# Optimization experiments

Measured on AMD Instinct MI355X. Metric: run time of the kernel, lower is better.

## Reference

```python
import jax, jax.numpy as jnp
import numpy as np

N, K, F = 16384, 64, 2048
ALPHA = 1.0
GAMMA = 1.0


def setup_inputs() -> dict:
    key = jax.random.key(0)
    k1, k2, k3, k4 = jax.random.split(key, 4)
    features = jax.random.normal(k1, (N, F), dtype=jnp.float32)
    idx = jax.random.randint(k2, (N,), 0, K)
    labels = jax.nn.one_hot(idx, K, dtype=jnp.float32)  # [N, K] one-hot
    # original initializes clusters to zeros (degenerate); use small random values
    cluster = jax.random.normal(k3, (K, F), dtype=jnp.float32) * 0.02
    class_weight = jax.random.uniform(k4, (K,), dtype=jnp.float32, minval=0.5, maxval=1.5)
    return {"features": features, "labels": labels, "cluster": cluster,
            "class_weight": class_weight}


def reference(features, labels, cluster, class_weight):
    # ci: cluster center of each sample's argmax label  [N, F]
    idx = jnp.argmax(labels, axis=1)
    ci = cluster[idx]
    # numerator: squared distance to own center  [N]
    nume = jnp.sum((features - ci) ** 2, axis=1)
    # denom: sum_j ||c_j - c_i||^2 + alpha  (TF flattens cj to [N, K*F] and
    # tiles ci K times; the squared norm over that axis is exactly this sum)
    d2 = jnp.sum((cluster[:, None, :] - cluster[None, :, :]) ** 2, axis=-1)  # [K, K]
    row_sum = jnp.sum(d2, axis=1)                                            # [K]
    denom = row_sum[idx] + ALPHA                                             # [N]
    loss = (nume / denom)[:, None]                                           # [N, 1]
    # cluster update: weighted_delta[k,f] = sum_n cw[n,k]*labels[n,k]*(x[n,f]-c[k,f])/denom[n]
    # with cw[n,k] = labels[n,k] * class_weight[k]. Expressed without the
    # [N,K,F] intermediates the TF code materializes:
    A = (labels * labels) * class_weight[None, :] / denom[:, None]  # [N, K]
    weighted_delta = jnp.einsum('nk,nf->kf', A, features) - jnp.sum(A, axis=0)[:, None] * cluster
    new_cluster = cluster - GAMMA * weighted_delta  # assign_sub side effect
    return loss, new_cluster
```

## Files before the change

kernel.cpp:

```cpp
#include <hip/hip_runtime.h>

#define NROWS 16384
#define KC 64
#define FDIM 2048
#define F4 (FDIM / 4)
#define ALPHA 1.0f
#define GAMMA 1.0f
#define ROWS_PER_BLK 32
#define HB 256
#define ROWS_PER_HB 64

typedef float f32x4 __attribute__((ext_vector_type(4)));

__global__ __launch_bounds__(256) void k_argmax_hist(
    const float* __restrict__ labels, int* __restrict__ idx,
    int* __restrict__ blockHist) {
    __shared__ int hist[KC];
    int t = threadIdx.x, w = t >> 6, lane = t & 63;
    if (t < KC) hist[t] = 0;
    __syncthreads();
    int rowbase = blockIdx.x * ROWS_PER_HB + w * 16;
    #pragma unroll
    for (int r0 = 0; r0 < 16; r0 += 4) {
        float v0 = labels[(rowbase + r0 + 0) * KC + lane];
        float v1 = labels[(rowbase + r0 + 1) * KC + lane];
        float v2 = labels[(rowbase + r0 + 2) * KC + lane];
        float v3 = labels[(rowbase + r0 + 3) * KC + lane];
        unsigned long long m0 = __ballot(v0 > 0.5f);
        unsigned long long m1 = __ballot(v1 > 0.5f);
        unsigned long long m2 = __ballot(v2 > 0.5f);
        unsigned long long m3 = __ballot(v3 > 0.5f);
        if (lane == 0) {
            int k0 = __ffsll(m0) - 1;
            int k1 = __ffsll(m1) - 1;
            int k2 = __ffsll(m2) - 1;
            int k3 = __ffsll(m3) - 1;
            idx[rowbase + r0 + 0] = k0;
            idx[rowbase + r0 + 1] = k1;
            idx[rowbase + r0 + 2] = k2;
            idx[rowbase + r0 + 3] = k3;
            atomicAdd(&hist[k0], 1);
            atomicAdd(&hist[k1], 1);
            atomicAdd(&hist[k2], 1);
            atomicAdd(&hist[k3], 1);
        }
    }
    __syncthreads();
    if (t < KC) blockHist[blockIdx.x * KC + t] = hist[t];
}

__global__ __launch_bounds__(64) void k_prefix(
    const int* __restrict__ blockHist, int* __restrict__ blockBase,
    int* __restrict__ counts, int* __restrict__ offsets) {
    int k = threadIdx.x;
    int acc = 0;
    for (int b = 0; b < HB; ++b) {
        int c = blockHist[b * KC + k];
        blockBase[b * KC + k] = acc;
        acc += c;
    }
    counts[k] = acc;
    __shared__ int tot[KC];
    tot[k] = acc;
    __syncthreads();
    if (k == 0) {
        int a = 0;
        for (int j = 0; j < KC; ++j) { offsets[j] = a; a += tot[j]; }
    }
}

__global__ __launch_bounds__(64) void k_scatter(
    const int* __restrict__ idx, const int* __restrict__ offsets,
    const int* __restrict__ blockBase, int* __restrict__ order) {
    __shared__ int cur[KC];
    int t = threadIdx.x;
    cur[t] = offsets[t] + blockBase[blockIdx.x * KC + t];
    __syncthreads();
    int n = blockIdx.x * ROWS_PER_HB + t;
    int k = idx[n];
    int p = atomicAdd(&cur[k], 1);
    order[p] = n;
}

__global__ __launch_bounds__(256) void k_rowsum(
    const float* __restrict__ cluster, const float* __restrict__ cw,
    float* __restrict__ inv_denom, float* __restrict__ scale) {
    int k = blockIdx.x, t = threadIdx.x;
    const float4* c4 = (const float4*)cluster;
    float4 a0 = c4[k * F4 + t];
    float4 a1 = c4[k * F4 + 256 + t];
    float acc = 0.f;
    for (int j = 0; j < KC; ++j) {
        float4 b0 = c4[j * F4 + t];
        float4 b1 = c4[j * F4 + 256 + t];
        float d;
        d = a0.x - b0.x; acc += d * d;
        d = a0.y - b0.y; acc += d * d;
        d = a0.z - b0.z; acc += d * d;
        d = a0.w - b0.w; acc += d * d;
        d = a1.x - b1.x; acc += d * d;
        d = a1.y - b1.y; acc += d * d;
        d = a1.z - b1.z; acc += d * d;
        d = a1.w - b1.w; acc += d * d;
    }
    #pragma unroll
    for (int off = 32; off >= 1; off >>= 1) acc += __shfl_down(acc, off);
    __shared__ float red[4];
    if ((t & 63) == 0) red[t >> 6] = acc;
    __syncthreads();
    if (t == 0) {
        float denom = red[0] + red[1] + red[2] + red[3] + ALPHA;
        inv_denom[k] = 1.0f / denom;
        scale[k]     = cw[k] / denom;
    }
}

__global__ __launch_bounds__(256) void k_main(
    const float* __restrict__ features, const float* __restrict__ cluster,
    const int* __restrict__ idx, const int* __restrict__ order,
    const float* __restrict__ inv_denom, float* __restrict__ delta,
    float* __restrict__ loss) {
    int t = threadIdx.x;
    __shared__ float part[ROWS_PER_BLK][256];
    __shared__ int onum[ROWS_PER_BLK];
    __shared__ int okk[ROWS_PER_BLK];
    int base = blockIdx.x * ROWS_PER_BLK;
    if (t < ROWS_PER_BLK) {
        int n = order[base + t];
        onum[t] = n;
        okk[t]  = idx[n];
    }
    __syncthreads();

    const f32x4* f4 = (const f32x4*)features;
    const float4* c4 = (const float4*)cluster;
    int cur_k = -1;
    float4 s0 = {0.f, 0.f, 0.f, 0.f}, s1 = {0.f, 0.f, 0.f, 0.f};
    float4 c0 = s0, c1 = s1;

    for (int r = 0; r < ROWS_PER_BLK; ++r) {
        int n = onum[r];
        int k = okk[r];
        if (k != cur_k) {
            if (cur_k >= 0) {
                float* dk = delta + cur_k * FDIM;
                atomicAdd(&dk[t * 4 + 0], s0.x);
                atomicAdd(&dk[t * 4 + 1], s0.y);
                atomicAdd(&dk[t * 4 + 2], s0.z);
                atomicAdd(&dk[t * 4 + 3], s0.w);
                atomicAdd(&dk[1024 + t * 4 + 0], s1.x);
                atomicAdd(&dk[1024 + t * 4 + 1], s1.y);
                atomicAdd(&dk[1024 + t * 4 + 2], s1.z);
                atomicAdd(&dk[1024 + t * 4 + 3], s1.w);
                s0.x = s0.y = s0.z = s0.w = 0.f;
                s1.x = s1.y = s1.z = s1.w = 0.f;
            }
            c0 = c4[k * F4 + t];
            c1 = c4[k * F4 + 256 + t];
            cur_k = k;
        }
        f32x4 xv0 = __builtin_nontemporal_load(&f4[(size_t)n * F4 + t]);
        f32x4 xv1 = __builtin_nontemporal_load(&f4[(size_t)n * F4 + 256 + t]);
        float4 x0 = {xv0.x, xv0.y, xv0.z, xv0.w};
        float4 x1 = {xv1.x, xv1.y, xv1.z, xv1.w};
        s0.x += x0.x; s0.y += x0.y; s0.z += x0.z; s0.w += x0.w;
        s1.x += x1.x; s1.y += x1.y; s1.z += x1.z; s1.w += x1.w;
        float d, p = 0.f;
        d = x0.x - c0.x; p += d * d;
        d = x0.y - c0.y; p += d * d;
        d = x0.z - c0.z; p += d * d;
        d = x0.w - c0.w; p += d * d;
        d = x1.x - c1.x; p += d * d;
        d = x1.y - c1.y; p += d * d;
        d = x1.z - c1.z; p += d * d;
        d = x1.w - c1.w; p += d * d;
        part[r][t] = p;
    }
    {
        float* dk = delta + cur_k * FDIM;
        atomicAdd(&dk[t * 4 + 0], s0.x);
        atomicAdd(&dk[t * 4 + 1], s0.y);
        atomicAdd(&dk[t * 4 + 2], s0.z);
        atomicAdd(&dk[t * 4 + 3], s0.w);
        atomicAdd(&dk[1024 + t * 4 + 0], s1.x);
        atomicAdd(&dk[1024 + t * 4 + 1], s1.y);
        atomicAdd(&dk[1024 + t * 4 + 2], s1.z);
        atomicAdd(&dk[1024 + t * 4 + 3], s1.w);
    }
    __syncthreads();
    int w = t >> 6, l = t & 63;
    for (int r = w; r < ROWS_PER_BLK; r += 4) {
        float v = part[r][l] + part[r][l + 64] + part[r][l + 128] + part[r][l + 192];
        #pragma unroll
        for (int off = 32; off >= 1; off >>= 1) v += __shfl_down(v, off);
        if (l == 0) {
            loss[onum[r]] = v * inv_denom[okk[r]];
        }
    }
}

__global__ __launch_bounds__(256) void k_finalize(
    const float* __restrict__ cluster, const float* __restrict__ delta,
    const int* __restrict__ counts, const float* __restrict__ scale,
    float* __restrict__ outc) {
    int e = blockIdx.x * 256 + threadIdx.x;
    int k = e >> 9;
    const float4* c4 = (const float4*)cluster;
    const float4* d4 = (const float4*)delta;
    float4 c = c4[e], d = d4[e];
    float s = scale[k], cnt = (float)counts[k];
    float4 o;
    o.x = c.x - GAMMA * s * (d.x - cnt * c.x);
    o.y = c.y - GAMMA * s * (d.y - cnt * c.y);
    o.z = c.z - GAMMA * s * (d.z - cnt * c.z);
    o.w = c.w - GAMMA * s * (d.w - cnt * c.w);
    ((float4*)outc)[e] = o;
}

extern "C" void kernel_launch(void* const* d_in, const int* in_sizes, int n_in,
                              void* d_out, int out_size, void* d_ws, size_t ws_size,
                              hipStream_t stream) {
    const float* features = (const float*)d_in[0];
    const float* labels   = (const float*)d_in[1];
    const float* cluster  = (const float*)d_in[2];
    const float* cw       = (const float*)d_in[3];
    float* loss = (float*)d_out;
    float* outc = (float*)d_out + NROWS;

    char*  ws        = (char*)d_ws;
    float* delta     = (float*)ws;
    int*   counts    = (int*)(ws + (size_t)KC * FDIM * 4);
    int*   offsets   = counts + KC;
    float* inv_denom = (float*)(offsets + KC);
    float* scale     = inv_denom + KC;
    int*   idx       = (int*)(scale + KC);
    int*   order     = idx + NROWS;
    int*   blockHist = order + NROWS;
    int*   blockBase = blockHist + HB * KC;

    hipMemsetAsync(delta, 0, (size_t)KC * FDIM * 4, stream);

    k_argmax_hist<<<HB, 256, 0, stream>>>(labels, idx, blockHist);
    k_rowsum<<<KC, 256, 0, stream>>>(cluster, cw, inv_denom, scale);
    k_prefix<<<1, 64, 0, stream>>>(blockHist, blockBase, counts, offsets);
    k_scatter<<<HB, 64, 0, stream>>>(idx, offsets, blockBase, order);
    k_main<<<NROWS / ROWS_PER_BLK, 256, 0, stream>>>(features, cluster, idx, order,
                                                     inv_denom, delta, loss);
    k_finalize<<<(KC * F4) / 256, 256, 0, stream>>>(cluster, delta, counts, scale, outc);
}
```

Baseline: 229.0 us.

## Split main kernel across feature halves, unroll uniform-cluster fast path, parallelize prefix

The main kernel now takes 16 rows per block and splits the feature dimension into two halves handled by separate blocks. This quadruples the grid, and per-row loss partials are combined with atomics into a zeroed loss buffer. A fast path for blocks whose rows all share one cluster unrolls four independent feature loads to raise memory-level parallelism. The single-wave prefix kernel is spread over four waves by chunking the block histogram. In exchange it adds a memset, loss atomics and twice as many delta atomic flushes.

```diff
diff --git a/kernel.cpp b/kernel.cpp
--- a/kernel.cpp
+++ b/kernel.cpp
@@ -6,7 +6,7 @@
 #define F4 (FDIM / 4)
 #define ALPHA 1.0f
 #define GAMMA 1.0f
-#define ROWS_PER_BLK 32
+#define ROWS 16
 #define HB 256
 #define ROWS_PER_HB 64
 
@@ -49,23 +49,33 @@
     if (t < KC) blockHist[blockIdx.x * KC + t] = hist[t];
 }
 
-__global__ __launch_bounds__(64) void k_prefix(
+__global__ __launch_bounds__(256) void k_prefix(
     const int* __restrict__ blockHist, int* __restrict__ blockBase,
     int* __restrict__ counts, int* __restrict__ offsets) {
-    int k = threadIdx.x;
+    int t = threadIdx.x;
+    int c = t >> 6;
+    int k = t & 63;
+    __shared__ int chunkTot[4][KC];
+    __shared__ int kTot[KC];
     int acc = 0;
-    for (int b = 0; b < HB; ++b) {
-        int c = blockHist[b * KC + k];
-        blockBase[b * KC + k] = acc;
-        acc += c;
-    }
-    counts[k] = acc;
-    __shared__ int tot[KC];
-    tot[k] = acc;
-    __syncthreads();
-    if (k == 0) {
+    for (int b = c * 64; b < c * 64 + 64; ++b) acc += blockHist[b * KC + k];
+    chunkTot[c][k] = acc;
+    __syncthreads();
+    if (c == 0) {
+        int tot = chunkTot[0][k] + chunkTot[1][k] + chunkTot[2][k] + chunkTot[3][k];
+        kTot[k] = tot;
+        counts[k] = tot;
+    }
+    __syncthreads();
+    if (t == 0) {
         int a = 0;
-        for (int j = 0; j < KC; ++j) { offsets[j] = a; a += tot[j]; }
+        for (int j = 0; j < KC; ++j) { offsets[j] = a; a += kTot[j]; }
+    }
+    int run = 0;
+    for (int cc = 0; cc < c; ++cc) run += chunkTot[cc][k];
+    for (int b = c * 64; b < c * 64 + 64; ++b) {
+        blockBase[b * KC + k] = run;
+        run += blockHist[b * KC + k];
     }
 }
 
@@ -121,80 +131,105 @@
     const float* __restrict__ inv_denom, float* __restrict__ delta,
     float* __restrict__ loss) {
     int t = threadIdx.x;
-    __shared__ float part[ROWS_PER_BLK][256];
-    __shared__ int onum[ROWS_PER_BLK];
-    __shared__ int okk[ROWS_PER_BLK];
-    int base = blockIdx.x * ROWS_PER_BLK;
-    if (t < ROWS_PER_BLK) {
-        int n = order[base + t];
+    int pair = blockIdx.x >> 1, half = blockIdx.x & 1;
+    int foff = half * 256;
+    __shared__ float part[ROWS][256];
+    __shared__ int onum[ROWS];
+    __shared__ int okk[ROWS];
+    if (t < ROWS) {
+        int n = order[pair * ROWS + t];
         onum[t] = n;
         okk[t]  = idx[n];
     }
     __syncthreads();
 
     const f32x4* f4 = (const f32x4*)features;
-    const float4* c4 = (const float4*)cluster;
-    int cur_k = -1;
-    float4 s0 = {0.f, 0.f, 0.f, 0.f}, s1 = {0.f, 0.f, 0.f, 0.f};
-    float4 c0 = s0, c1 = s1;
-
-    for (int r = 0; r < ROWS_PER_BLK; ++r) {
-        int n = onum[r];
-        int k = okk[r];
-        if (k != cur_k) {
-            if (cur_k >= 0) {
-                float* dk = delta + cur_k * FDIM;
-                atomicAdd(&dk[t * 4 + 0], s0.x);
-                atomicAdd(&dk[t * 4 + 1], s0.y);
-                atomicAdd(&dk[t * 4 + 2], s0.z);
-                atomicAdd(&dk[t * 4 + 3], s0.w);
-                atomicAdd(&dk[1024 + t * 4 + 0], s1.x);
-                atomicAdd(&dk[1024 + t * 4 + 1], s1.y);
-                atomicAdd(&dk[1024 + t * 4 + 2], s1.z);
-                atomicAdd(&dk[1024 + t * 4 + 3], s1.w);
-                s0.x = s0.y = s0.z = s0.w = 0.f;
-                s1.x = s1.y = s1.z = s1.w = 0.f;
+    const f32x4* c4 = (const f32x4*)cluster;
+    float4 s = {0.f, 0.f, 0.f, 0.f};
+    int k0 = okk[0];
+
+    if (okk[ROWS - 1] == k0) {
+        f32x4 cv = c4[k0 * F4 + foff + t];
+        for (int r = 0; r < ROWS; r += 4) {
+            f32x4 x0 = __builtin_nontemporal_load(&f4[(size_t)onum[r + 0] * F4 + foff + t]);
+            f32x4 x1 = __builtin_nontemporal_load(&f4[(size_t)onum[r + 1] * F4 + foff + t]);
+            f32x4 x2 = __builtin_nontemporal_load(&f4[(size_t)onum[r + 2] * F4 + foff + t]);
+            f32x4 x3 = __builtin_nontemporal_load(&f4[(size_t)onum[r + 3] * F4 + foff + t]);
+            float d, p;
+            s.x += x0.x; s.y += x0.y; s.z += x0.z; s.w += x0.w;
+            p = 0.f;
+            d = x0.x - cv.x; p += d * d;
+            d = x0.y - cv.y; p += d * d;
+            d = x0.z - cv.z; p += d * d;
+            d = x0.w - cv.w; p += d * d;
+            part[r + 0][t] = p;
+            s.x += x1.x; s.y += x1.y; s.z += x1.z; s.w += x1.w;
+            p = 0.f;
+            d = x1.x - cv.x; p += d * d;
+            d = x1.y - cv.y; p += d * d;
+            d = x1.z - cv.z; p += d * d;
+            d = x1.w - cv.w; p += d * d;
+            part[r + 1][t] = p;
+            s.x += x2.x; s.y += x2.y; s.z += x2.z; s.w += x2.w;
+            p = 0.f;
+            d = x2.x - cv.x; p += d * d;
+            d = x2.y - cv.y; p += d * d;
+            d = x2.z - cv.z; p += d * d;
+            d = x2.w - cv.w; p += d * d;
+            part[r + 2][t] = p;
+            s.x += x3.x; s.y += x3.y; s.z += x3.z; s.w += x3.w;
+            p = 0.f;
+            d = x3.x - cv.x; p += d * d;
+            d = x3.y - cv.y; p += d * d;
+            d = x3.z - cv.z; p += d * d;
+            d = x3.w - cv.w; p += d * d;
+            part[r + 3][t] = p;
+        }
+        float* dk = delta + k0 * FDIM + half * 1024;
+        atomicAdd(&dk[t * 4 + 0], s.x);
+        atomicAdd(&dk[t * 4 + 1], s.y);
+        atomicAdd(&dk[t * 4 + 2], s.z);
+        atomicAdd(&dk[t * 4 + 3], s.w);
+    } else {
+        int cur_k = -1;
+        f32x4 cv;
+        for (int r = 0; r < ROWS; ++r) {
+            int k = okk[r];
+            if (k != cur_k) {
+                if (cur_k >= 0) {
+                    float* dk = delta + cur_k * FDIM + half * 1024;
+                    atomicAdd(&dk[t * 4 + 0], s.x);
+                    atomicAdd(&dk[t * 4 + 1], s.y);
+                    atomicAdd(&dk[t * 4 + 2], s.z);
+                    atomicAdd(&dk[t * 4 + 3], s.w);
+                    s.x = s.y = s.z = s.w = 0.f;
+                }
+                cv = c4[k * F4 + foff + t];
+                cur_k = k;
             }
-            c0 = c4[k * F4 + t];
-            c1 = c4[k * F4 + 256 + t];
-            cur_k = k;
-        }
-        f32x4 xv0 = __builtin_nontemporal_load(&f4[(size_t)n * F4 + t]);
-        f32x4 xv1 = __builtin_nontemporal_load(&f4[(size_t)n * F4 + 256 + t]);
-        float4 x0 = {xv0.x, xv0.y, xv0.z, xv0.w};
-        float4 x1 = {xv1.x, xv1.y, xv1.z, xv1.w};
-        s0.x += x0.x; s0.y += x0.y; s0.z += x0.z; s0.w += x0.w;
-        s1.x += x1.x; s1.y += x1.y; s1.z += x1.z; s1.w += x1.w;
-        float d, p = 0.f;
-        d = x0.x - c0.x; p += d * d;
-        d = x0.y - c0.y; p += d * d;
-        d = x0.z - c0.z; p += d * d;
-        d = x0.w - c0.w; p += d * d;
-        d = x1.x - c1.x; p += d * d;
-        d = x1.y - c1.y; p += d * d;
-        d = x1.z - c1.z; p += d * d;
-        d = x1.w - c1.w; p += d * d;
-        part[r][t] = p;
-    }
-    {
-        float* dk = delta + cur_k * FDIM;
-        atomicAdd(&dk[t * 4 + 0], s0.x);
-        atomicAdd(&dk[t * 4 + 1], s0.y);
-        atomicAdd(&dk[t * 4 + 2], s0.z);
-        atomicAdd(&dk[t * 4 + 3], s0.w);
-        atomicAdd(&dk[1024 + t * 4 + 0], s1.x);
-        atomicAdd(&dk[1024 + t * 4 + 1], s1.y);
-        atomicAdd(&dk[1024 + t * 4 + 2], s1.z);
-        atomicAdd(&dk[1024 + t * 4 + 3], s1.w);
+            f32x4 x = __builtin_nontemporal_load(&f4[(size_t)onum[r] * F4 + foff + t]);
+            s.x += x.x; s.y += x.y; s.z += x.z; s.w += x.w;
+            float d, p = 0.f;
+            d = x.x - cv.x; p += d * d;
+            d = x.y - cv.y; p += d * d;
+            d = x.z - cv.z; p += d * d;
+            d = x.w - cv.w; p += d * d;
+            part[r][t] = p;
+        }
+        float* dk = delta + cur_k * FDIM + half * 1024;
+        atomicAdd(&dk[t * 4 + 0], s.x);
+        atomicAdd(&dk[t * 4 + 1], s.y);
+        atomicAdd(&dk[t * 4 + 2], s.z);
+        atomicAdd(&dk[t * 4 + 3], s.w);
     }
     __syncthreads();
     int w = t >> 6, l = t & 63;
-    for (int r = w; r < ROWS_PER_BLK; r += 4) {
+    for (int r = w; r < ROWS; r += 4) {
         float v = part[r][l] + part[r][l + 64] + part[r][l + 128] + part[r][l + 192];
         #pragma unroll
         for (int off = 32; off >= 1; off >>= 1) v += __shfl_down(v, off);
         if (l == 0) {
-            loss[onum[r]] = v * inv_denom[okk[r]];
+            atomicAdd(&loss[onum[r]], v * inv_denom[okk[r]]);
         }
     }
 }
@@ -239,12 +274,13 @@
     int*   blockBase = blockHist + HB * KC;
 
     hipMemsetAsync(delta, 0, (size_t)KC * FDIM * 4, stream);
+    hipMemsetAsync(loss, 0, (size_t)NROWS * 4, stream);
 
     k_argmax_hist<<<HB, 256, 0, stream>>>(labels, idx, blockHist);
     k_rowsum<<<KC, 256, 0, stream>>>(cluster, cw, inv_denom, scale);
-    k_prefix<<<1, 64, 0, stream>>>(blockHist, blockBase, counts, offsets);
+    k_prefix<<<1, 256, 0, stream>>>(blockHist, blockBase, counts, offsets);
     k_scatter<<<HB, 64, 0, stream>>>(idx, offsets, blockBase, order);
-    k_main<<<NROWS / ROWS_PER_BLK, 256, 0, stream>>>(features, cluster, idx, order,
-                                                     inv_denom, delta, loss);
+    k_main<<<(NROWS / ROWS) * 2, 256, 0, stream>>>(features, cluster, idx, order,
+                                                   inv_denom, delta, loss);
     k_finalize<<<(KC * F4) / 256, 256, 0, stream>>>(cluster, delta, counts, scale, outc);
 }
```

Result: slower. 237.8 us (+3.9%).
